# Kernel optimization log

Measured on AMD Instinct MI355X. Metric: run time of the kernel, lower is better.

## Reference

```python
import jax, jax.numpy as jnp
import numpy as np

NUM_EXPERTS = 16
HIDDEN = 1024
INTERMEDIATE = 4096
TOTAL_TOKENS = 32768  # 2048 tokens per expert


def setup_inputs() -> dict:
    key = jax.random.key(0)
    k1, k2, k3 = jax.random.split(key, 3)
    hidden_states = jax.random.normal(k1, (TOTAL_TOKENS, HIDDEN), dtype=jnp.float32)
    gate_up_proj = jax.random.normal(k2, (NUM_EXPERTS, HIDDEN, 2 * INTERMEDIATE), dtype=jnp.float32)
    down_proj = jax.random.normal(k3, (NUM_EXPERTS, INTERMEDIATE, HIDDEN), dtype=jnp.float32)
    return {"hidden_states": hidden_states, "gate_up_proj": gate_up_proj, "down_proj": down_proj}


def reference(hidden_states, gate_up_proj, down_proj):
    E, H = gate_up_proj.shape[0], gate_up_proj.shape[1]
    # (E, T, H): tokens pre-grouped by expert, as in the torch module's reshape
    x = hidden_states.reshape(E, -1, H)
    # batched expert GEMM: (E,T,H) @ (E,H,2I) -> (E,T,2I)
    gate_up = jnp.einsum('eth,ehf->etf', x, gate_up_proj)
    gate, up = jnp.split(gate_up, 2, axis=-1)
    gated = up * jax.nn.silu(gate)  # SwiGLU
    # down projection: (E,T,I) @ (E,I,H) -> (E,T,H)
    out = jnp.einsum('eti,eih->eth', gated, down_proj)
    return out.reshape(-1, H)
```

## Files before the change

### kernel.cpp

```cpp
#include <hip/hip_runtime.h>
#include <hip/hip_bf16.h>
#include <cstdint>
#include <cstddef>

#define NE  16
#define HD  1024
#define ID  4096
#define TPE 2048
#define TOKENS 32768

typedef __attribute__((ext_vector_type(8))) short short8;
typedef __attribute__((ext_vector_type(4))) float f32x4;
typedef __attribute__((ext_vector_type(4))) unsigned short u16x4;
typedef __attribute__((ext_vector_type(8))) unsigned short u16x8;

static __device__ __forceinline__ unsigned short f2b(float f) {
    __bf16 h = (__bf16)f;
    return __builtin_bit_cast(unsigned short, h);
}

#define GLOAD16(gsrc, ldsbase)                                                  \
    __builtin_amdgcn_global_load_lds(                                           \
        (const __attribute__((address_space(1))) unsigned int*)(gsrc),          \
        (__attribute__((address_space(3))) unsigned int*)(ldsbase), 16, 0, 0)

#define MFMA16(a, b, c) __builtin_amdgcn_mfma_f32_16x16x32_bf16((a), (b), (c), 0, 0, 0)

__global__ void k_f2b(const float* __restrict__ src, unsigned short* __restrict__ dst, int n4)
{
    int i = blockIdx.x * blockDim.x + threadIdx.x;
    int stride = gridDim.x * blockDim.x;
    for (; i < n4; i += stride) {
        float4 v = *(const float4*)(src + (size_t)i * 4);
        u16x4 b = { f2b(v.x), f2b(v.y), f2b(v.z), f2b(v.w) };
        *(u16x4*)(dst + (size_t)i * 4) = b;
    }
}

__global__ __launch_bounds__(256) void k_transpose(const float* __restrict__ src,
                                                   unsigned short* __restrict__ dst,
                                                   int K, int N, int e0)
{
    __shared__ unsigned short LT[64][72];
    const int t  = threadIdx.x;
    const int eL = blockIdx.z;
    const float* s = src + (size_t)(e0 + eL) * K * N
                         + (size_t)(blockIdx.y * 64) * N + blockIdx.x * 64;
    unsigned short* d = dst + (size_t)eL * N * K
                            + (size_t)(blockIdx.x * 64) * K + blockIdx.y * 64;
    #pragma unroll
    for (int i = 0; i < 4; ++i) {
        int row = i * 16 + (t >> 4);
        int c4  = (t & 15) * 4;
        float4 v = *(const float4*)(s + (size_t)row * N + c4);
        LT[c4 + 0][row] = f2b(v.x);
        LT[c4 + 1][row] = f2b(v.y);
        LT[c4 + 2][row] = f2b(v.z);
        LT[c4 + 3][row] = f2b(v.w);
    }
    __syncthreads();
    #pragma unroll
    for (int i = 0; i < 2; ++i) {
        int n  = i * 32 + (t >> 3);
        int k8 = (t & 7) * 8;
        u16x8 v = *(const u16x8*)&LT[n][k8];
        *(u16x8*)(d + (size_t)n * K + k8) = v;
    }
}

__global__ __launch_bounds__(512, 2) void k_gemm1(const unsigned short* __restrict__ hsB,
                                                  const unsigned short* __restrict__ gupT,
                                                  unsigned short* __restrict__ gated,
                                                  int e0)
{
    __shared__ unsigned short As[2][256 * 64];
    __shared__ unsigned short Bs[2][256 * 64];
    const int NT = HD / 64;

    const int t    = threadIdx.x;
    const int lane = t & 63;
    const int w    = t >> 6;
    const int wr   = w >> 2;
    const int wc   = w & 3;
    const int eL   = blockIdx.z;
    const int e    = e0 + eL;
    const int n0g  = blockIdx.x * 128;
    const int m0   = blockIdx.y * 256;

    const unsigned short* gA  = hsB  + (size_t)(e * TPE + m0) * HD;
    const unsigned short* gBt = gupT + (size_t)eL * (2 * ID) * HD;

    f32x4 acc[8][4];
    #pragma unroll
    for (int i = 0; i < 8; ++i)
        #pragma unroll
        for (int j = 0; j < 4; ++j)
            acc[i][j] = f32x4{0.f, 0.f, 0.f, 0.f};

    auto STAGE = [&](int buf, int kt) {
        #pragma unroll
        for (int i = 0; i < 4; ++i) {
            int idx = i * 512 + t;
            int row = idx >> 3, sl = idx & 7;
            GLOAD16(gA + (size_t)row * HD + kt * 64 + ((sl ^ (row & 7)) << 3),
                    &As[buf][(size_t)(i * 512 + (t & ~63)) * 8]);
        }
        #pragma unroll
        for (int i = 0; i < 4; ++i) {
            int idx = i * 512 + t;
            int c = idx >> 3, sl = idx & 7;
            int g = c >> 5, j = c & 31;
            int grow = ((g & 1) ? ID : 0) + n0g + ((g >> 1) << 5) + (c & 31);
            (void)j;
            GLOAD16(gBt + (size_t)grow * HD + kt * 64 + ((sl ^ (c & 7)) << 3),
                    &Bs[buf][(size_t)(i * 512 + (t & ~63)) * 8]);
        }
    };

    short8 avP[8], bvP[4], avQ[8], bvQ[4];

    auto READ_A = [&](const unsigned short* Ab, int ks, short8* av) {
        #pragma unroll
        for (int f = 0; f < 8; ++f) {
            int row = wr * 128 + f * 16 + (lane & 15);
            int sl  = ks * 4 + (lane >> 4);
            av[f] = *(const short8*)&Ab[row * 64 + ((sl ^ (row & 7)) << 3)];
        }
    };
    auto READ_B = [&](const unsigned short* Bb, int ks, short8* bv) {
        #pragma unroll
        for (int fn = 0; fn < 4; ++fn) {
            int c  = wc * 64 + fn * 16 + (lane & 15);
            int sl = ks * 4 + (lane >> 4);
            bv[fn] = *(const short8*)&Bb[c * 64 + ((sl ^ (c & 7)) << 3)];
        }
    };

    STAGE(0, 0);
    STAGE(1, 1);
    asm volatile("s_waitcnt vmcnt(8)" ::: "memory");
    __builtin_amdgcn_s_barrier();
    READ_A(&As[0][0], 0, avP);  READ_B(&Bs[0][0], 0, bvP);

    for (int kt = 0; kt < NT; ++kt) {
        const int cur = kt & 1;
        const unsigned short* Ab  = &As[cur][0];
        const unsigned short* Bb  = &Bs[cur][0];
        const unsigned short* Abn = &As[cur ^ 1][0];
        const unsigned short* Bbn = &Bs[cur ^ 1][0];
        const int ktn2 = (kt + 2 < NT) ? kt + 2 : NT - 1;

        READ_A(Ab, 1, avQ);  READ_B(Bb, 1, bvQ);
        asm volatile("s_waitcnt lgkmcnt(12)" ::: "memory");
        __builtin_amdgcn_sched_barrier(0);
        __builtin_amdgcn_s_setprio(1);
        #pragma unroll
        for (int f = 0; f < 8; ++f)
            #pragma unroll
            for (int fn = 0; fn < 4; ++fn)
                acc[f][fn] = MFMA16(avP[f], bvP[fn], acc[f][fn]);
        __builtin_amdgcn_s_setprio(0);

        asm volatile("s_waitcnt lgkmcnt(0)" ::: "memory");
        __builtin_amdgcn_s_barrier();
        STAGE(cur, ktn2);
        asm volatile("s_waitcnt vmcnt(8)" ::: "memory");
        __builtin_amdgcn_s_barrier();
        __builtin_amdgcn_sched_barrier(0);

        READ_A(Abn, 0, avP);  READ_B(Bbn, 0, bvP);

        __builtin_amdgcn_s_setprio(1);
        #pragma unroll
        for (int f = 0; f < 8; ++f)
            #pragma unroll
            for (int fn = 0; fn < 4; ++fn)
                acc[f][fn] = MFMA16(avQ[f], bvQ[fn], acc[f][fn]);
        __builtin_amdgcn_s_setprio(0);
    }
    asm volatile("s_waitcnt vmcnt(0)" ::: "memory");

    unsigned short* g0 = gated + ((size_t)eL * TPE + m0) * ID;
    const int rq = (lane >> 4) << 2;
    const int cl = lane & 15;
    #pragma unroll
    for (int fm = 0; fm < 8; ++fm) {
        #pragma unroll
        for (int fp = 0; fp < 2; ++fp) {
            f32x4 g = acc[fm][fp];
            f32x4 u = acc[fm][fp + 2];
            #pragma unroll
            for (int r = 0; r < 4; ++r) {
                float gv  = g[r];
                float val = u[r] * gv / (1.0f + __expf(-gv));
                int row = wr * 128 + fm * 16 + rq + r;
                int col = n0g + wc * 32 + fp * 16 + cl;
                g0[(size_t)row * ID + col] = f2b(val);
            }
        }
    }
}

__global__ __launch_bounds__(512, 2) void k_gemm2(const unsigned short* __restrict__ gated,
                                                  const unsigned short* __restrict__ dwnT,
                                                  float* __restrict__ out,
                                                  int e0)
{
    __shared__ unsigned short As[2][256 * 64];
    __shared__ unsigned short Bs[2][256 * 64];
    const int NT = ID / 64;

    const int t    = threadIdx.x;
    const int lane = t & 63;
    const int w    = t >> 6;
    const int wr   = w >> 2;
    const int wc   = w & 3;
    const int eL   = blockIdx.z;
    const int e    = e0 + eL;
    const int n0   = blockIdx.x * 256;
    const int m0   = blockIdx.y * 256;

    const unsigned short* gA  = gated + ((size_t)eL * TPE + m0) * ID;
    const unsigned short* gBt = dwnT  + (size_t)eL * HD * ID;

    f32x4 acc[8][4];
    #pragma unroll
    for (int i = 0; i < 8; ++i)
        #pragma unroll
        for (int j = 0; j < 4; ++j)
            acc[i][j] = f32x4{0.f, 0.f, 0.f, 0.f};

    auto STAGE = [&](int buf, int kt) {
        #pragma unroll
        for (int i = 0; i < 4; ++i) {
            int idx = i * 512 + t;
            int row = idx >> 3, sl = idx & 7;
            GLOAD16(gA + (size_t)row * ID + kt * 64 + ((sl ^ (row & 7)) << 3),
                    &As[buf][(size_t)(i * 512 + (t & ~63)) * 8]);
        }
        #pragma unroll
        for (int i = 0; i < 4; ++i) {
            int idx = i * 512 + t;
            int c = idx >> 3, sl = idx & 7;
            GLOAD16(gBt + (size_t)(n0 + c) * ID + kt * 64 + ((sl ^ (c & 7)) << 3),
                    &Bs[buf][(size_t)(i * 512 + (t & ~63)) * 8]);
        }
    };

    short8 avP[8], bvP[4], avQ[8], bvQ[4];

    auto READ_A = [&](const unsigned short* Ab, int ks, short8* av) {
        #pragma unroll
        for (int f = 0; f < 8; ++f) {
            int row = wr * 128 + f * 16 + (lane & 15);
            int sl  = ks * 4 + (lane >> 4);
            av[f] = *(const short8*)&Ab[row * 64 + ((sl ^ (row & 7)) << 3)];
        }
    };
    auto READ_B = [&](const unsigned short* Bb, int ks, short8* bv) {
        #pragma unroll
        for (int fn = 0; fn < 4; ++fn) {
            int c  = wc * 64 + fn * 16 + (lane & 15);
            int sl = ks * 4 + (lane >> 4);
            bv[fn] = *(const short8*)&Bb[c * 64 + ((sl ^ (c & 7)) << 3)];
        }
    };

    STAGE(0, 0);
    STAGE(1, 1);
    asm volatile("s_waitcnt vmcnt(8)" ::: "memory");
    __builtin_amdgcn_s_barrier();
    READ_A(&As[0][0], 0, avP);  READ_B(&Bs[0][0], 0, bvP);

    for (int kt = 0; kt < NT; ++kt) {
        const int cur = kt & 1;
        const unsigned short* Ab  = &As[cur][0];
        const unsigned short* Bb  = &Bs[cur][0];
        const unsigned short* Abn = &As[cur ^ 1][0];
        const unsigned short* Bbn = &Bs[cur ^ 1][0];
        const int ktn2 = (kt + 2 < NT) ? kt + 2 : NT - 1;

        READ_A(Ab, 1, avQ);  READ_B(Bb, 1, bvQ);
        asm volatile("s_waitcnt lgkmcnt(12)" ::: "memory");
        __builtin_amdgcn_sched_barrier(0);
        __builtin_amdgcn_s_setprio(1);
        #pragma unroll
        for (int f = 0; f < 8; ++f)
            #pragma unroll
            for (int fn = 0; fn < 4; ++fn)
                acc[f][fn] = MFMA16(avP[f], bvP[fn], acc[f][fn]);
        __builtin_amdgcn_s_setprio(0);

        asm volatile("s_waitcnt lgkmcnt(0)" ::: "memory");
        __builtin_amdgcn_s_barrier();
        STAGE(cur, ktn2);
        asm volatile("s_waitcnt vmcnt(8)" ::: "memory");
        __builtin_amdgcn_s_barrier();
        __builtin_amdgcn_sched_barrier(0);

        READ_A(Abn, 0, avP);  READ_B(Bbn, 0, bvP);

        __builtin_amdgcn_s_setprio(1);
        #pragma unroll
        for (int f = 0; f < 8; ++f)
            #pragma unroll
            for (int fn = 0; fn < 4; ++fn)
                acc[f][fn] = MFMA16(avQ[f], bvQ[fn], acc[f][fn]);
        __builtin_amdgcn_s_setprio(0);
    }
    asm volatile("s_waitcnt vmcnt(0)" ::: "memory");

    float* o0 = out + (size_t)(e * TPE + m0) * HD;
    const int rq = (lane >> 4) << 2;
    const int cl = lane & 15;
    #pragma unroll
    for (int fm = 0; fm < 8; ++fm) {
        #pragma unroll
        for (int fn = 0; fn < 4; ++fn) {
            #pragma unroll
            for (int r = 0; r < 4; ++r) {
                int row = wr * 128 + fm * 16 + rq + r;
                int col = n0 + wc * 64 + fn * 16 + cl;
                o0[(size_t)row * HD + col] = acc[fm][fn][r];
            }
        }
    }
}

extern "C" void kernel_launch(void* const* d_in, const int* in_sizes, int n_in,
                              void* d_out, int out_size, void* d_ws, size_t ws_size,
                              hipStream_t stream)
{
    (void)in_sizes; (void)n_in; (void)out_size;
    const float* hs  = (const float*)d_in[0];
    const float* gup = (const float*)d_in[1];
    const float* dwn = (const float*)d_in[2];
    float* out = (float*)d_out;

    const size_t SZ_HSB   = (size_t)TOKENS * HD * 2;
    const size_t SZ_GUPT  = (size_t)2 * ID * HD * 2;
    const size_t SZ_DWNT  = (size_t)HD * ID * 2;
    const size_t SZ_GATED = (size_t)TPE * ID * 2;
    const size_t perExp   = SZ_GUPT + SZ_DWNT + SZ_GATED;

    int G = (ws_size > SZ_HSB) ? (int)((ws_size - SZ_HSB) / perExp) : 1;
    if (G < 1) G = 1;
    if (G > NE) G = NE;

    unsigned short* hsB   = (unsigned short*)d_ws;
    unsigned short* gupT  = (unsigned short*)((char*)d_ws + SZ_HSB);
    unsigned short* dwnT  = (unsigned short*)((char*)d_ws + SZ_HSB + (size_t)G * SZ_GUPT);
    unsigned short* gated = (unsigned short*)((char*)d_ws + SZ_HSB + (size_t)G * (SZ_GUPT + SZ_DWNT));

    k_f2b<<<2048, 256, 0, stream>>>(hs, hsB, TOKENS * HD / 4);

    for (int e0 = 0; e0 < NE; e0 += G) {
        int ne = NE - e0;
        if (ne > G) ne = G;
        k_transpose<<<dim3((2 * ID) / 64, HD / 64, ne), 256, 0, stream>>>(gup, gupT, HD, 2 * ID, e0);
        k_transpose<<<dim3(HD / 64, ID / 64, ne), 256, 0, stream>>>(dwn, dwnT, ID, HD, e0);
        k_gemm1<<<dim3(ID / 128, TPE / 256, ne), 512, 0, stream>>>(hsB, gupT, gated, e0);
        k_gemm2<<<dim3(HD / 256, TPE / 256, ne), 512, 0, stream>>>(gated, dwnT, out, e0);
    }
}
```

Measured before the change: 1.284 ms.

## Split GEMM mainloop into four quadrant phases with interleaved half-tile staging

Restructures both expert GEMM main loops into an 8-wave ping-pong style schedule. Each k-tile is split into four MFMA quadrants (A half × B half), and each quadrant's LDS reads and global-to-LDS loads are scheduled between barriers. Staging is now split into half tiles per A/B row group, so loads for the next tiles overlap with compute on the current one. The aim is better overlap of memory traffic and LDS reads with MFMA issue. The cost is more barriers per iteration and a more fragile buffer-reuse ordering.

```diff
diff --git a/kernel.cpp b/kernel.cpp
--- a/kernel.cpp
+++ b/kernel.cpp
@@ -68,6 +68,84 @@
     }
 }
 
+
+#define GEMM_BODY(READ_A_HALF, READ_B_HALF, STAGE_A, STAGE_B, NT)               \
+    STAGE_A(0, 0, 0);  STAGE_B(0, 0, 0);  STAGE_B(0, 0, 1);  STAGE_A(0, 0, 1); \
+    STAGE_A(1, 1, 0);  STAGE_B(1, 1, 0);  STAGE_B(1, 1, 1);                     \
+    asm volatile("s_waitcnt vmcnt(6)" ::: "memory");        \
+    __builtin_amdgcn_s_barrier();                                               \
+    for (int kt = 0; kt < NT; ++kt) {                                           \
+        const int cur = kt & 1, nxt = cur ^ 1;                                  \
+        const int ktn  = (kt + 1 < NT) ? kt + 1 : NT - 1;                       \
+        const int ktn2 = (kt + 2 < NT) ? kt + 2 : NT - 1;                       \
+        short8 avA[8], bvB0[4], bvB1[4];                                        \
+                                                    \
+        READ_A_HALF(cur, 0, avA);                                               \
+        READ_B_HALF(cur, 0, bvB0);                                              \
+        STAGE_A(nxt, ktn, 1);                                                   \
+        asm volatile("s_waitcnt lgkmcnt(8)" ::: "memory");                      \
+        __builtin_amdgcn_s_barrier();                                           \
+        asm volatile("s_waitcnt lgkmcnt(0)" ::: "memory");                      \
+        __builtin_amdgcn_sched_barrier(0);                                      \
+        __builtin_amdgcn_s_setprio(1);                                          \
+        _Pragma("unroll")                                                       \
+        for (int f = 0; f < 4; ++f)                                             \
+            _Pragma("unroll")                                                   \
+            for (int j = 0; j < 2; ++j)                                         \
+                _Pragma("unroll")                                               \
+                for (int ks = 0; ks < 2; ++ks)                                  \
+                    acc[f][j] = MFMA16(avA[f * 2 + ks], bvB0[j * 2 + ks], acc[f][j]); \
+        __builtin_amdgcn_s_setprio(0);                                          \
+        __builtin_amdgcn_s_barrier();                                           \
+                                                    \
+        READ_B_HALF(cur, 1, bvB1);                                              \
+        STAGE_A(cur, ktn2, 0);                                                  \
+        __builtin_amdgcn_s_barrier();                                           \
+        asm volatile("s_waitcnt lgkmcnt(0)" ::: "memory");                      \
+        __builtin_amdgcn_sched_barrier(0);                                      \
+        __builtin_amdgcn_s_setprio(1);                                          \
+        _Pragma("unroll")                                                       \
+        for (int f = 0; f < 4; ++f)                                             \
+            _Pragma("unroll")                                                   \
+            for (int j = 0; j < 2; ++j)                                         \
+                _Pragma("unroll")                                               \
+                for (int ks = 0; ks < 2; ++ks)                                  \
+                    acc[f][2 + j] = MFMA16(avA[f * 2 + ks], bvB1[j * 2 + ks], acc[f][2 + j]); \
+        __builtin_amdgcn_s_setprio(0);                                          \
+        __builtin_amdgcn_s_barrier();                                           \
+                                                    \
+        READ_A_HALF(cur, 1, avA);                                               \
+        STAGE_B(cur, ktn2, 0);                                                  \
+        __builtin_amdgcn_s_barrier();                                           \
+        asm volatile("s_waitcnt lgkmcnt(0)" ::: "memory");                      \
+        __builtin_amdgcn_sched_barrier(0);                                      \
+        __builtin_amdgcn_s_setprio(1);                                          \
+        _Pragma("unroll")                                                       \
+        for (int f = 0; f < 4; ++f)                                             \
+            _Pragma("unroll")                                                   \
+            for (int j = 0; j < 2; ++j)                                         \
+                _Pragma("unroll")                                               \
+                for (int ks = 0; ks < 2; ++ks)                                  \
+                    acc[4 + f][j] = MFMA16(avA[f * 2 + ks], bvB0[j * 2 + ks], acc[4 + f][j]); \
+        __builtin_amdgcn_s_setprio(0);                                          \
+        __builtin_amdgcn_s_barrier();                                           \
+                                                    \
+        STAGE_B(cur, ktn2, 1);                                                  \
+        __builtin_amdgcn_s_barrier();                                           \
+        __builtin_amdgcn_s_setprio(1);                                          \
+        _Pragma("unroll")                                                       \
+        for (int f = 0; f < 4; ++f)                                             \
+            _Pragma("unroll")                                                   \
+            for (int j = 0; j < 2; ++j)                                         \
+                _Pragma("unroll")                                               \
+                for (int ks = 0; ks < 2; ++ks)                                  \
+                    acc[4 + f][2 + j] = MFMA16(avA[f * 2 + ks], bvB1[j * 2 + ks], acc[4 + f][2 + j]); \
+        __builtin_amdgcn_s_setprio(0);                                          \
+        asm volatile("s_waitcnt vmcnt(6)" ::: "memory");   \
+        __builtin_amdgcn_s_barrier();                                           \
+    }                                                                           \
+    asm volatile("s_waitcnt vmcnt(0)" ::: "memory");
+
 __global__ __launch_bounds__(512, 2) void k_gemm1(const unsigned short* __restrict__ hsB,
                                                   const unsigned short* __restrict__ gupT,
                                                   unsigned short* __restrict__ gated,
@@ -75,7 +153,6 @@
 {
     __shared__ unsigned short As[2][256 * 64];
     __shared__ unsigned short Bs[2][256 * 64];
-    const int NT = HD / 64;
 
     const int t    = threadIdx.x;
     const int lane = t & 63;
@@ -97,88 +174,52 @@
         for (int j = 0; j < 4; ++j)
             acc[i][j] = f32x4{0.f, 0.f, 0.f, 0.f};
 
-    auto STAGE = [&](int buf, int kt) {
-        #pragma unroll
-        for (int i = 0; i < 4; ++i) {
-            int idx = i * 512 + t;
-            int row = idx >> 3, sl = idx & 7;
+    auto STAGE_A = [&](int buf, int kt, int I) {
+        #pragma unroll
+        for (int i = 0; i < 2; ++i) {
+            int m  = i * 8 + w;
+            int r0 = ((m >> 3) * 128) + ((m & 7) * 8) + I * 64;
+            int row = r0 + (lane >> 3);
+            int sl  = lane & 7;
             GLOAD16(gA + (size_t)row * HD + kt * 64 + ((sl ^ (row & 7)) << 3),
-                    &As[buf][(size_t)(i * 512 + (t & ~63)) * 8]);
-        }
-        #pragma unroll
-        for (int i = 0; i < 4; ++i) {
-            int idx = i * 512 + t;
-            int c = idx >> 3, sl = idx & 7;
-            int g = c >> 5, j = c & 31;
+                    &As[buf][r0 * 64]);
+        }
+    };
+    auto STAGE_B = [&](int buf, int kt, int J) {
+        #pragma unroll
+        for (int i = 0; i < 2; ++i) {
+            int m  = i * 8 + w;
+            int c0 = ((m >> 2) * 64) + ((m & 3) * 8) + J * 32;
+            int c  = c0 + (lane >> 3);
+            int sl = lane & 7;
+            int g  = c >> 5;
             int grow = ((g & 1) ? ID : 0) + n0g + ((g >> 1) << 5) + (c & 31);
-            (void)j;
             GLOAD16(gBt + (size_t)grow * HD + kt * 64 + ((sl ^ (c & 7)) << 3),
-                    &Bs[buf][(size_t)(i * 512 + (t & ~63)) * 8]);
-        }
-    };
-
-    short8 avP[8], bvP[4], avQ[8], bvQ[4];
-
-    auto READ_A = [&](const unsigned short* Ab, int ks, short8* av) {
-        #pragma unroll
-        for (int f = 0; f < 8; ++f) {
-            int row = wr * 128 + f * 16 + (lane & 15);
-            int sl  = ks * 4 + (lane >> 4);
-            av[f] = *(const short8*)&Ab[row * 64 + ((sl ^ (row & 7)) << 3)];
-        }
-    };
-    auto READ_B = [&](const unsigned short* Bb, int ks, short8* bv) {
-        #pragma unroll
-        for (int fn = 0; fn < 4; ++fn) {
-            int c  = wc * 64 + fn * 16 + (lane & 15);
-            int sl = ks * 4 + (lane >> 4);
-            bv[fn] = *(const short8*)&Bb[c * 64 + ((sl ^ (c & 7)) << 3)];
-        }
-    };
-
-    STAGE(0, 0);
-    STAGE(1, 1);
-    asm volatile("s_waitcnt vmcnt(8)" ::: "memory");
-    __builtin_amdgcn_s_barrier();
-    READ_A(&As[0][0], 0, avP);  READ_B(&Bs[0][0], 0, bvP);
-
-    for (int kt = 0; kt < NT; ++kt) {
-        const int cur = kt & 1;
-        const unsigned short* Ab  = &As[cur][0];
-        const unsigned short* Bb  = &Bs[cur][0];
-        const unsigned short* Abn = &As[cur ^ 1][0];
-        const unsigned short* Bbn = &Bs[cur ^ 1][0];
-        const int ktn2 = (kt + 2 < NT) ? kt + 2 : NT - 1;
-
-        READ_A(Ab, 1, avQ);  READ_B(Bb, 1, bvQ);
-        asm volatile("s_waitcnt lgkmcnt(12)" ::: "memory");
-        __builtin_amdgcn_sched_barrier(0);
-        __builtin_amdgcn_s_setprio(1);
-        #pragma unroll
-        for (int f = 0; f < 8; ++f)
-            #pragma unroll
-            for (int fn = 0; fn < 4; ++fn)
-                acc[f][fn] = MFMA16(avP[f], bvP[fn], acc[f][fn]);
-        __builtin_amdgcn_s_setprio(0);
-
-        asm volatile("s_waitcnt lgkmcnt(0)" ::: "memory");
-        __builtin_amdgcn_s_barrier();
-        STAGE(cur, ktn2);
-        asm volatile("s_waitcnt vmcnt(8)" ::: "memory");
-        __builtin_amdgcn_s_barrier();
-        __builtin_amdgcn_sched_barrier(0);
-
-        READ_A(Abn, 0, avP);  READ_B(Bbn, 0, bvP);
-
-        __builtin_amdgcn_s_setprio(1);
-        #pragma unroll
-        for (int f = 0; f < 8; ++f)
-            #pragma unroll
-            for (int fn = 0; fn < 4; ++fn)
-                acc[f][fn] = MFMA16(avQ[f], bvQ[fn], acc[f][fn]);
-        __builtin_amdgcn_s_setprio(0);
-    }
-    asm volatile("s_waitcnt vmcnt(0)" ::: "memory");
+                    &Bs[buf][c0 * 64]);
+        }
+    };
+    auto READ_A_HALF = [&](int buf, int I, short8* av) {
+        #pragma unroll
+        for (int f = 0; f < 4; ++f)
+            #pragma unroll
+            for (int ks = 0; ks < 2; ++ks) {
+                int row = wr * 128 + I * 64 + f * 16 + (lane & 15);
+                int sl  = ks * 4 + (lane >> 4);
+                av[f * 2 + ks] = *(const short8*)&As[buf][row * 64 + ((sl ^ (row & 7)) << 3)];
+            }
+    };
+    auto READ_B_HALF = [&](int buf, int J, short8* bv) {
+        #pragma unroll
+        for (int j = 0; j < 2; ++j)
+            #pragma unroll
+            for (int ks = 0; ks < 2; ++ks) {
+                int c  = wc * 64 + (J * 2 + j) * 16 + (lane & 15);
+                int sl = ks * 4 + (lane >> 4);
+                bv[j * 2 + ks] = *(const short8*)&Bs[buf][c * 64 + ((sl ^ (c & 7)) << 3)];
+            }
+    };
+
+    GEMM_BODY(READ_A_HALF, READ_B_HALF, STAGE_A, STAGE_B, (HD / 64))
 
     unsigned short* g0 = gated + ((size_t)eL * TPE + m0) * ID;
     const int rq = (lane >> 4) << 2;
@@ -208,7 +249,6 @@
 {
     __shared__ unsigned short As[2][256 * 64];
     __shared__ unsigned short Bs[2][256 * 64];
-    const int NT = ID / 64;
 
     const int t    = threadIdx.x;
     const int lane = t & 63;
@@ -230,85 +270,50 @@
         for (int j = 0; j < 4; ++j)
             acc[i][j] = f32x4{0.f, 0.f, 0.f, 0.f};
 
-    auto STAGE = [&](int buf, int kt) {
-        #pragma unroll
-        for (int i = 0; i < 4; ++i) {
-            int idx = i * 512 + t;
-            int row = idx >> 3, sl = idx & 7;
+    auto STAGE_A = [&](int buf, int kt, int I) {
+        #pragma unroll
+        for (int i = 0; i < 2; ++i) {
+            int m  = i * 8 + w;
+            int r0 = ((m >> 3) * 128) + ((m & 7) * 8) + I * 64;
+            int row = r0 + (lane >> 3);
+            int sl  = lane & 7;
             GLOAD16(gA + (size_t)row * ID + kt * 64 + ((sl ^ (row & 7)) << 3),
-                    &As[buf][(size_t)(i * 512 + (t & ~63)) * 8]);
-        }
-        #pragma unroll
-        for (int i = 0; i < 4; ++i) {
-            int idx = i * 512 + t;
-            int c = idx >> 3, sl = idx & 7;
+                    &As[buf][r0 * 64]);
+        }
+    };
+    auto STAGE_B = [&](int buf, int kt, int J) {
+        #pragma unroll
+        for (int i = 0; i < 2; ++i) {
+            int m  = i * 8 + w;
+            int c0 = ((m >> 2) * 64) + ((m & 3) * 8) + J * 32;
+            int c  = c0 + (lane >> 3);
+            int sl = lane & 7;
             GLOAD16(gBt + (size_t)(n0 + c) * ID + kt * 64 + ((sl ^ (c & 7)) << 3),
-                    &Bs[buf][(size_t)(i * 512 + (t & ~63)) * 8]);
-        }
-    };
-
-    short8 avP[8], bvP[4], avQ[8], bvQ[4];
-
-    auto READ_A = [&](const unsigned short* Ab, int ks, short8* av) {
-        #pragma unroll
-        for (int f = 0; f < 8; ++f) {
-            int row = wr * 128 + f * 16 + (lane & 15);
-            int sl  = ks * 4 + (lane >> 4);
-            av[f] = *(const short8*)&Ab[row * 64 + ((sl ^ (row & 7)) << 3)];
-        }
-    };
-    auto READ_B = [&](const unsigned short* Bb, int ks, short8* bv) {
-        #pragma unroll
-        for (int fn = 0; fn < 4; ++fn) {
-            int c  = wc * 64 + fn * 16 + (lane & 15);
-            int sl = ks * 4 + (lane >> 4);
-            bv[fn] = *(const short8*)&Bb[c * 64 + ((sl ^ (c & 7)) << 3)];
-        }
-    };
-
-    STAGE(0, 0);
-    STAGE(1, 1);
-    asm volatile("s_waitcnt vmcnt(8)" ::: "memory");
-    __builtin_amdgcn_s_barrier();
-    READ_A(&As[0][0], 0, avP);  READ_B(&Bs[0][0], 0, bvP);
-
-    for (int kt = 0; kt < NT; ++kt) {
-        const int cur = kt & 1;
-        const unsigned short* Ab  = &As[cur][0];
-        const unsigned short* Bb  = &Bs[cur][0];
-        const unsigned short* Abn = &As[cur ^ 1][0];
-        const unsigned short* Bbn = &Bs[cur ^ 1][0];
-        const int ktn2 = (kt + 2 < NT) ? kt + 2 : NT - 1;
-
-        READ_A(Ab, 1, avQ);  READ_B(Bb, 1, bvQ);
-        asm volatile("s_waitcnt lgkmcnt(12)" ::: "memory");
-        __builtin_amdgcn_sched_barrier(0);
-        __builtin_amdgcn_s_setprio(1);
-        #pragma unroll
-        for (int f = 0; f < 8; ++f)
-            #pragma unroll
-            for (int fn = 0; fn < 4; ++fn)
-                acc[f][fn] = MFMA16(avP[f], bvP[fn], acc[f][fn]);
-        __builtin_amdgcn_s_setprio(0);
-
-        asm volatile("s_waitcnt lgkmcnt(0)" ::: "memory");
-        __builtin_amdgcn_s_barrier();
-        STAGE(cur, ktn2);
-        asm volatile("s_waitcnt vmcnt(8)" ::: "memory");
-        __builtin_amdgcn_s_barrier();
-        __builtin_amdgcn_sched_barrier(0);
-
-        READ_A(Abn, 0, avP);  READ_B(Bbn, 0, bvP);
-
-        __builtin_amdgcn_s_setprio(1);
-        #pragma unroll
-        for (int f = 0; f < 8; ++f)
-            #pragma unroll
-            for (int fn = 0; fn < 4; ++fn)
-                acc[f][fn] = MFMA16(avQ[f], bvQ[fn], acc[f][fn]);
-        __builtin_amdgcn_s_setprio(0);
-    }
-    asm volatile("s_waitcnt vmcnt(0)" ::: "memory");
+                    &Bs[buf][c0 * 64]);
+        }
+    };
+    auto READ_A_HALF = [&](int buf, int I, short8* av) {
+        #pragma unroll
+        for (int f = 0; f < 4; ++f)
+            #pragma unroll
+            for (int ks = 0; ks < 2; ++ks) {
+                int row = wr * 128 + I * 64 + f * 16 + (lane & 15);
+                int sl  = ks * 4 + (lane >> 4);
+                av[f * 2 + ks] = *(const short8*)&As[buf][row * 64 + ((sl ^ (row & 7)) << 3)];
+            }
+    };
+    auto READ_B_HALF = [&](int buf, int J, short8* bv) {
+        #pragma unroll
+        for (int j = 0; j < 2; ++j)
+            #pragma unroll
+            for (int ks = 0; ks < 2; ++ks) {
+                int c  = wc * 64 + (J * 2 + j) * 16 + (lane & 15);
+                int sl = ks * 4 + (lane >> 4);
+                bv[j * 2 + ks] = *(const short8*)&Bs[buf][c * 64 + ((sl ^ (c & 7)) << 3)];
+            }
+    };
+
+    GEMM_BODY(READ_A_HALF, READ_B_HALF, STAGE_A, STAGE_B, (ID / 64))
 
     float* o0 = out + (size_t)(e * TPE + m0) * HD;
     const int rq = (lane >> 4) << 2;
```

After: 1.295 ms. No clear change (+0.9%).
